# Performance work log

Hardware: AMD Instinct MI355X
Metric: run time of the kernel (lower is better)

Reference implementation:

```python
import jax, jax.numpy as jnp
import numpy as np

RC = 6.0            # cosine cutoff radius (Angstrom)
N_ANGULAR = 128     # module init arg; output dim = 3*N_ANGULAR
EPS = 1e-12


def cosine_cutoff(d):
    # Behler-style cosine cutoff: 0.5*(cos(pi*d/rc)+1) for d < rc, else 0
    return jnp.where(d < RC, 0.5 * (jnp.cos(jnp.pi * d / RC) + 1.0), 0.0)


def setup_inputs() -> dict:
    key = jax.random.key(0)
    k1, k2, k3, k4 = jax.random.split(key, 4)
    B, N, M = 8, 4096, 96
    L = 20.0  # box length
    positions = jax.random.uniform(k1, (B, N, 3), dtype=jnp.float32) * L
    cell = jnp.tile(jnp.eye(3, dtype=jnp.float32) * L, (B, 1, 1))
    neighbors = jax.random.randint(k2, (B, N, M), 0, N, dtype=jnp.int32)
    offsets = jax.random.randint(k3, (B, N, M, 3), -1, 2).astype(jnp.float32)
    mask = (jax.random.uniform(k4, (B, N, M)) > 0.1).astype(jnp.float32)
    return {"positions": positions, "cell": cell, "offsets": offsets,
            "mask": mask, "neighbors": neighbors}


def reference(positions, cell, offsets, mask, neighbors):
    B, N, M = neighbors.shape
    # gather neighbor positions: pos_j[b,n,m,:] = positions[b, neighbors[b,n,m], :]
    idx = neighbors.reshape(B, N * M)
    pos_j = jnp.take_along_axis(positions, idx[:, :, None], axis=1).reshape(B, N, M, 3)
    # displacement vectors with periodic offsets (offsets in cell coordinates)
    dis_vec = pos_j - positions[:, :, None, :] + jnp.einsum('bnmi,bij->bnmj', offsets, cell)
    distances = jnp.sqrt(jnp.sum(dis_vec * dis_vec, axis=-1) + EPS)  # [B,N,M]
    # cutoff / distance, zeroed where mask == 0
    cut = jnp.where(mask != 0.0, cosine_cutoff(distances) / distances, 0.0)
    # sort neighbors by descending cut value, gather cut-weighted vectors in that order
    order = jnp.argsort(-cut, axis=-1)                       # [B,N,M]
    cut_vec = cut[..., None] * dis_vec                       # [B,N,M,3]
    cut_vec = jnp.take_along_axis(cut_vec, order[..., None], axis=2)
    cut_vec = cut_vec.reshape(B, N, M * 3)
    # scatter into zero-padded descriptor of width 3*n_angular
    f = jnp.zeros((B, N, N_ANGULAR * 3), dtype=positions.dtype)
    f = f.at[:, :, : M * 3].set(cut_vec)
    return f
```

## Files before the change

kernel.cpp:

```cpp
#include <hip/hip_runtime.h>
#include <math.h>

#define M_NB   96
#define OUT_W  384
#define NATOM  4096
#define WPB    16
#define NITER  4

__global__ __launch_bounds__(64 * WPB, 8) void deepmd_angular_kernel(
    const float* __restrict__ positions,
    const float* __restrict__ cell,
    const float* __restrict__ offsets,
    const float* __restrict__ mask,
    const int*   __restrict__ neighbors,
    float*       __restrict__ out,
    int N)
{
    __shared__ float pos_s[NATOM * 3];
    __shared__ float cut_s[WPB][M_NB];

    const int tid  = threadIdx.x;
    const int wv   = tid >> 6;
    const int lane = tid & 63;
    const bool low = lane < 32;

    const int p0 = blockIdx.x * (WPB * NITER);
    const int b  = p0 / N;

    {
        const float4* src = (const float4*)(positions + (size_t)b * N * 3);
        float4* dst = (float4*)pos_s;
        const int nf4 = (N * 3) >> 2;
        #pragma unroll
        for (int i = tid; i < nf4; i += 64 * WPB) dst[i] = src[i];
    }
    __syncthreads();

    const float* cb = cell + (size_t)b * 9;
    const float c00 = cb[0], c01 = cb[1], c02 = cb[2];
    const float c10 = cb[3], c11 = cb[4], c12 = cb[5];
    const float c20 = cb[6], c21 = cb[7], c22 = cb[8];

    const float4 z4 = make_float4(0.f, 0.f, 0.f, 0.f);
    const float2 z2 = make_float2(0.f, 0.f);

    #pragma unroll
    for (int it = 0; it < NITER; ++it) {
        const int q  = p0 + wv * NITER + it;
        const int nn = q - b * N;

        float* rowp = out + (size_t)q * OUT_W;
        ((float4*)rowp)[lane] = z4;
        ((float2*)(rowp + 256))[lane] = z2;

        const long eA = (long)q * M_NB + lane;
        const int   jA  = neighbors[eA];
        const float mkA = mask[eA];
        const float oA0 = offsets[eA * 3], oA1 = offsets[eA * 3 + 1], oA2 = offsets[eA * 3 + 2];

        int jB = 0; float mkB = 0.f, oB0 = 0.f, oB1 = 0.f, oB2 = 0.f;
        if (low) {
            const long eB = eA + 64;
            jB  = neighbors[eB];
            mkB = mask[eB];
            oB0 = offsets[eB * 3]; oB1 = offsets[eB * 3 + 1]; oB2 = offsets[eB * 3 + 2];
        }

        const float pix = pos_s[nn * 3 + 0];
        const float piy = pos_s[nn * 3 + 1];
        const float piz = pos_s[nn * 3 + 2];

        const float axA = pos_s[jA * 3 + 0], ayA = pos_s[jA * 3 + 1], azA = pos_s[jA * 3 + 2];

        const float dxA = axA - pix + oA0 * c00 + oA1 * c10 + oA2 * c20;
        const float dyA = ayA - piy + oA0 * c01 + oA1 * c11 + oA2 * c21;
        const float dzA = azA - piz + oA0 * c02 + oA1 * c12 + oA2 * c22;
        const float dA  = sqrtf(dxA * dxA + dyA * dyA + dzA * dzA + 1e-12f);
        float cutA = 0.f;
        if (mkA != 0.f && dA < 6.f)
            cutA = 0.5f * (cosf(dA * 0.52359877559829887f) + 1.f) / dA;

        float dxB = 0.f, dyB = 0.f, dzB = 0.f, cutB = 0.f;
        if (low) {
            const float axB = pos_s[jB * 3 + 0], ayB = pos_s[jB * 3 + 1], azB = pos_s[jB * 3 + 2];
            dxB = axB - pix + oB0 * c00 + oB1 * c10 + oB2 * c20;
            dyB = ayB - piy + oB0 * c01 + oB1 * c11 + oB2 * c21;
            dzB = azB - piz + oB0 * c02 + oB1 * c12 + oB2 * c22;
            const float dB = sqrtf(dxB * dxB + dyB * dyB + dzB * dzB + 1e-12f);
            if (mkB != 0.f && dB < 6.f)
                cutB = 0.5f * (cosf(dB * 0.52359877559829887f) + 1.f) / dB;
        }

        cut_s[wv][lane] = cutA;
        if (low) cut_s[wv][64 + lane] = cutB;

        if (cutA != 0.f || cutB != 0.f) {
            __threadfence_block();
            if (cutA != 0.f) {
                const int mA = lane;
                int rank = 0;
                const float4* c4 = (const float4*)cut_s[wv];
                #pragma unroll
                for (int k4 = 0; k4 < M_NB / 4; ++k4) {
                    const float4 c = c4[k4];
                    const int k = 4 * k4;
                    rank += (c.x > cutA) || (c.x == cutA && k + 0 < mA);
                    rank += (c.y > cutA) || (c.y == cutA && k + 1 < mA);
                    rank += (c.z > cutA) || (c.z == cutA && k + 2 < mA);
                    rank += (c.w > cutA) || (c.w == cutA && k + 3 < mA);
                }
                rowp[rank * 3 + 0] = cutA * dxA;
                rowp[rank * 3 + 1] = cutA * dyA;
                rowp[rank * 3 + 2] = cutA * dzA;
            }
            if (low && cutB != 0.f) {
                const int mB = 64 + lane;
                int rank = 0;
                const float4* c4 = (const float4*)cut_s[wv];
                #pragma unroll
                for (int k4 = 0; k4 < M_NB / 4; ++k4) {
                    const float4 c = c4[k4];
                    const int k = 4 * k4;
                    rank += (c.x > cutB) || (c.x == cutB && k + 0 < mB);
                    rank += (c.y > cutB) || (c.y == cutB && k + 1 < mB);
                    rank += (c.z > cutB) || (c.z == cutB && k + 2 < mB);
                    rank += (c.w > cutB) || (c.w == cutB && k + 3 < mB);
                }
                rowp[rank * 3 + 0] = cutB * dxB;
                rowp[rank * 3 + 1] = cutB * dyB;
                rowp[rank * 3 + 2] = cutB * dzB;
            }
        }
    }
}

extern "C" void kernel_launch(void* const* d_in, const int* in_sizes, int n_in,
                              void* d_out, int out_size, void* d_ws, size_t ws_size,
                              hipStream_t stream) {
    const float* positions = (const float*)d_in[0];
    const float* cell      = (const float*)d_in[1];
    const float* offsets   = (const float*)d_in[2];
    const float* mask      = (const float*)d_in[3];
    const int*   neighbors = (const int*)d_in[4];
    float*       out       = (float*)d_out;

    const int BN = in_sizes[0] / 3;
    const int B  = in_sizes[1] / 9;
    const int N  = BN / B;

    dim3 block(64 * WPB, 1, 1);
    dim3 grid(BN / (WPB * NITER), 1, 1);
    deepmd_angular_kernel<<<grid, block, 0, stream>>>(
        positions, cell, offsets, mask, neighbors, out, N);
}
```

Before: 123.0 us.

## Assemble output rows in registers via wave shuffles instead of scattered stores

Instead of zeroing each output row and then scattering rank-ordered triples with scalar stores, every wave now broadcasts each active neighbor's rank and weighted vector through shuffles. Each lane merges the values that land in its float4 and float2 slots, and the row is written once with coalesced stores. Positions are also repacked into float4 in shared memory so one aligned LDS read fetches each gather, and offsets are loaded as float3. The price is a serial ballot loop of up to 96 iterations, each with four shuffles and compare chains, in place of about three scattered stores per lane.

```diff
diff --git a/kernel.cpp b/kernel.cpp
--- a/kernel.cpp
+++ b/kernel.cpp
@@ -6,6 +6,24 @@
 #define NATOM  4096
 #define WPB    16
 #define NITER  4
+
+__device__ __forceinline__ void merge3(float4& a4, float2& a2, int base,
+                                       float v0, float v1, float v2, int lane)
+{
+    const int f4lo = 4 * lane;
+    const int f2lo = 256 + 2 * lane;
+    const float v[3] = {v0, v1, v2};
+    #pragma unroll
+    for (int t = 0; t < 3; ++t) {
+        const int idx = base + t;
+        if      (idx == f4lo)     a4.x = v[t];
+        else if (idx == f4lo + 1) a4.y = v[t];
+        else if (idx == f4lo + 2) a4.z = v[t];
+        else if (idx == f4lo + 3) a4.w = v[t];
+        else if (idx == f2lo)     a2.x = v[t];
+        else if (idx == f2lo + 1) a2.y = v[t];
+    }
+}
 
 __global__ __launch_bounds__(64 * WPB, 8) void deepmd_angular_kernel(
     const float* __restrict__ positions,
@@ -16,8 +34,8 @@
     float*       __restrict__ out,
     int N)
 {
-    __shared__ float pos_s[NATOM * 3];
-    __shared__ float cut_s[WPB][M_NB];
+    __shared__ float4 pos4_s[NATOM];
+    __shared__ float  cut_s[WPB][M_NB];
 
     const int tid  = threadIdx.x;
     const int wv   = tid >> 6;
@@ -28,11 +46,11 @@
     const int b  = p0 / N;
 
     {
-        const float4* src = (const float4*)(positions + (size_t)b * N * 3);
-        float4* dst = (float4*)pos_s;
-        const int nf4 = (N * 3) >> 2;
-        #pragma unroll
-        for (int i = tid; i < nf4; i += 64 * WPB) dst[i] = src[i];
+        const float* pb_ = positions + (size_t)b * N * 3;
+        for (int a = tid; a < NATOM; a += 64 * WPB) {
+            const float3 v = *(const float3*)(pb_ + 3 * a);
+            pos4_s[a] = make_float4(v.x, v.y, v.z, 0.f);
+        }
     }
     __syncthreads();
 
@@ -41,40 +59,30 @@
     const float c10 = cb[3], c11 = cb[4], c12 = cb[5];
     const float c20 = cb[6], c21 = cb[7], c22 = cb[8];
 
-    const float4 z4 = make_float4(0.f, 0.f, 0.f, 0.f);
-    const float2 z2 = make_float2(0.f, 0.f);
-
     #pragma unroll
     for (int it = 0; it < NITER; ++it) {
         const int q  = p0 + wv * NITER + it;
         const int nn = q - b * N;
 
-        float* rowp = out + (size_t)q * OUT_W;
-        ((float4*)rowp)[lane] = z4;
-        ((float2*)(rowp + 256))[lane] = z2;
+        const long eA = (long)q * M_NB + lane;
+        const int    jA = neighbors[eA];
+        const float mkA = mask[eA];
+        const float3 oA = *(const float3*)(offsets + eA * 3);
 
-        const long eA = (long)q * M_NB + lane;
-        const int   jA  = neighbors[eA];
-        const float mkA = mask[eA];
-        const float oA0 = offsets[eA * 3], oA1 = offsets[eA * 3 + 1], oA2 = offsets[eA * 3 + 2];
-
-        int jB = 0; float mkB = 0.f, oB0 = 0.f, oB1 = 0.f, oB2 = 0.f;
+        int jB = 0; float mkB = 0.f; float3 oB = make_float3(0.f, 0.f, 0.f);
         if (low) {
             const long eB = eA + 64;
             jB  = neighbors[eB];
             mkB = mask[eB];
-            oB0 = offsets[eB * 3]; oB1 = offsets[eB * 3 + 1]; oB2 = offsets[eB * 3 + 2];
+            oB  = *(const float3*)(offsets + eB * 3);
         }
 
-        const float pix = pos_s[nn * 3 + 0];
-        const float piy = pos_s[nn * 3 + 1];
-        const float piz = pos_s[nn * 3 + 2];
+        const float4 pi  = pos4_s[nn];
+        const float4 pjA = pos4_s[jA];
 
-        const float axA = pos_s[jA * 3 + 0], ayA = pos_s[jA * 3 + 1], azA = pos_s[jA * 3 + 2];
-
-        const float dxA = axA - pix + oA0 * c00 + oA1 * c10 + oA2 * c20;
-        const float dyA = ayA - piy + oA0 * c01 + oA1 * c11 + oA2 * c21;
-        const float dzA = azA - piz + oA0 * c02 + oA1 * c12 + oA2 * c22;
+        const float dxA = pjA.x - pi.x + oA.x * c00 + oA.y * c10 + oA.z * c20;
+        const float dyA = pjA.y - pi.y + oA.x * c01 + oA.y * c11 + oA.z * c21;
+        const float dzA = pjA.z - pi.z + oA.x * c02 + oA.y * c12 + oA.z * c22;
         const float dA  = sqrtf(dxA * dxA + dyA * dyA + dzA * dzA + 1e-12f);
         float cutA = 0.f;
         if (mkA != 0.f && dA < 6.f)
@@ -82,10 +90,10 @@
 
         float dxB = 0.f, dyB = 0.f, dzB = 0.f, cutB = 0.f;
         if (low) {
-            const float axB = pos_s[jB * 3 + 0], ayB = pos_s[jB * 3 + 1], azB = pos_s[jB * 3 + 2];
-            dxB = axB - pix + oB0 * c00 + oB1 * c10 + oB2 * c20;
-            dyB = ayB - piy + oB0 * c01 + oB1 * c11 + oB2 * c21;
-            dzB = azB - piz + oB0 * c02 + oB1 * c12 + oB2 * c22;
+            const float4 pjB = pos4_s[jB];
+            dxB = pjB.x - pi.x + oB.x * c00 + oB.y * c10 + oB.z * c20;
+            dyB = pjB.y - pi.y + oB.x * c01 + oB.y * c11 + oB.z * c21;
+            dzB = pjB.z - pi.z + oB.x * c02 + oB.y * c12 + oB.z * c22;
             const float dB = sqrtf(dxB * dxB + dyB * dyB + dzB * dzB + 1e-12f);
             if (mkB != 0.f && dB < 6.f)
                 cutB = 0.5f * (cosf(dB * 0.52359877559829887f) + 1.f) / dB;
@@ -94,43 +102,63 @@
         cut_s[wv][lane] = cutA;
         if (low) cut_s[wv][64 + lane] = cutB;
 
-        if (cutA != 0.f || cutB != 0.f) {
-            __threadfence_block();
-            if (cutA != 0.f) {
-                const int mA = lane;
-                int rank = 0;
-                const float4* c4 = (const float4*)cut_s[wv];
-                #pragma unroll
-                for (int k4 = 0; k4 < M_NB / 4; ++k4) {
-                    const float4 c = c4[k4];
-                    const int k = 4 * k4;
-                    rank += (c.x > cutA) || (c.x == cutA && k + 0 < mA);
-                    rank += (c.y > cutA) || (c.y == cutA && k + 1 < mA);
-                    rank += (c.z > cutA) || (c.z == cutA && k + 2 < mA);
-                    rank += (c.w > cutA) || (c.w == cutA && k + 3 < mA);
-                }
-                rowp[rank * 3 + 0] = cutA * dxA;
-                rowp[rank * 3 + 1] = cutA * dyA;
-                rowp[rank * 3 + 2] = cutA * dzA;
+        int rkA = 0; float w0A = 0.f, w1A = 0.f, w2A = 0.f;
+        if (cutA != 0.f) {
+            const int mA = lane;
+            int rank = 0;
+            const float4* c4 = (const float4*)cut_s[wv];
+            #pragma unroll
+            for (int k4 = 0; k4 < M_NB / 4; ++k4) {
+                const float4 c = c4[k4];
+                const int k = 4 * k4;
+                rank += (c.x > cutA) || (c.x == cutA && k + 0 < mA);
+                rank += (c.y > cutA) || (c.y == cutA && k + 1 < mA);
+                rank += (c.z > cutA) || (c.z == cutA && k + 2 < mA);
+                rank += (c.w > cutA) || (c.w == cutA && k + 3 < mA);
             }
-            if (low && cutB != 0.f) {
-                const int mB = 64 + lane;
-                int rank = 0;
-                const float4* c4 = (const float4*)cut_s[wv];
-                #pragma unroll
-                for (int k4 = 0; k4 < M_NB / 4; ++k4) {
-                    const float4 c = c4[k4];
-                    const int k = 4 * k4;
-                    rank += (c.x > cutB) || (c.x == cutB && k + 0 < mB);
-                    rank += (c.y > cutB) || (c.y == cutB && k + 1 < mB);
-                    rank += (c.z > cutB) || (c.z == cutB && k + 2 < mB);
-                    rank += (c.w > cutB) || (c.w == cutB && k + 3 < mB);
-                }
-                rowp[rank * 3 + 0] = cutB * dxB;
-                rowp[rank * 3 + 1] = cutB * dyB;
-                rowp[rank * 3 + 2] = cutB * dzB;
+            rkA = rank; w0A = cutA * dxA; w1A = cutA * dyA; w2A = cutA * dzA;
+        }
+        int rkB = 0; float w0B = 0.f, w1B = 0.f, w2B = 0.f;
+        if (low && cutB != 0.f) {
+            const int mB = 64 + lane;
+            int rank = 0;
+            const float4* c4 = (const float4*)cut_s[wv];
+            #pragma unroll
+            for (int k4 = 0; k4 < M_NB / 4; ++k4) {
+                const float4 c = c4[k4];
+                const int k = 4 * k4;
+                rank += (c.x > cutB) || (c.x == cutB && k + 0 < mB);
+                rank += (c.y > cutB) || (c.y == cutB && k + 1 < mB);
+                rank += (c.z > cutB) || (c.z == cutB && k + 2 < mB);
+                rank += (c.w > cutB) || (c.w == cutB && k + 3 < mB);
             }
+            rkB = rank; w0B = cutB * dxB; w1B = cutB * dyB; w2B = cutB * dzB;
         }
+
+        unsigned long long bmA = __ballot(cutA != 0.f);
+        unsigned long long bmB = __ballot(low && cutB != 0.f);
+        float4 a4 = make_float4(0.f, 0.f, 0.f, 0.f);
+        float2 a2 = make_float2(0.f, 0.f);
+        while (bmA) {
+            const int src = (int)__builtin_ctzll(bmA); bmA &= bmA - 1;
+            const int   r  = __shfl(rkA, src);
+            const float v0 = __shfl(w0A, src);
+            const float v1 = __shfl(w1A, src);
+            const float v2 = __shfl(w2A, src);
+            merge3(a4, a2, 3 * r, v0, v1, v2, lane);
+        }
+        while (bmB) {
+            const int src = (int)__builtin_ctzll(bmB); bmB &= bmB - 1;
+            const int   r  = __shfl(rkB, src);
+            const float v0 = __shfl(w0B, src);
+            const float v1 = __shfl(w1B, src);
+            const float v2 = __shfl(w2B, src);
+            merge3(a4, a2, 3 * r, v0, v1, v2, lane);
+        }
+
+        float* rowp = out + (size_t)q * OUT_W;
+        ((float4*)rowp)[lane] = a4;
+        ((float2*)(rowp + 256))[lane] = a2;
     }
 }
 
```

Measured after the change: 123.1 us. Within noise of the previous version (+0.1%).
